# Performance work log

Measured on AMD Instinct MI355X. Metric: run time of the kernel, lower is better.

## Reference

```python
import jax, jax.numpy as jnp
import numpy as np
import math

T = 4096      # 2 s @ 2048 Hz (G2Net)
B = 64
NV = 16
SR = 2048.0
FLOW = 20.0
FHIGH = 512.0


def _build_wft():
    """Morlet-like wavelet filter bank in the frequency domain, exactly as in build()."""
    max_scale = T // (np.sqrt(2) * 2)
    if max_scale <= 1:
        max_scale = T // 2
    max_scale = np.floor(NV * np.log2(max_scale))
    scales = 2 * (2 ** (1 / NV)) ** np.arange(0, max_scale + 1)
    frequencies = SR * (6 / (2 * np.pi)) / scales
    frequencies = frequencies[frequencies >= FLOW]
    scales = scales[0:len(frequencies)]
    frequencies = frequencies[frequencies <= FHIGH]
    scales = scales[len(scales) - len(frequencies):len(scales)]
    padvalue = T // 2
    n = padvalue * 2 + T
    omega = np.arange(1, math.floor(n / 2) + 1, dtype=np.float64)
    omega = omega * (2 * np.pi) / n
    omega = np.concatenate((np.array([0.0]), omega,
                            -omega[np.arange(math.floor((n - 1) / 2), 0, -1, dtype=int) - 1]))
    wft = np.zeros([scales.size, omega.size])
    for jj, scale in enumerate(scales):
        expnt = -(scale * omega - 6) ** 2 / 2 * (omega > 0)
        wft[jj, :] = 2 * np.exp(expnt) * (omega > 0)
    return wft.astype(np.float32)  # [num_scales=75, n=8192]


def setup_inputs() -> dict:
    key = jax.random.key(0)
    inputs = jax.random.normal(key, (B, T), dtype=jnp.float32)
    wft = jnp.asarray(_build_wft())
    return {"inputs": inputs, "wft": wft}


def reference(inputs, wft):
    # inputs: [B, T] float32; wft: [S, n] float32 (n = 2*T)
    t = inputs.shape[1]
    pad = t // 2
    # symmetric (endpoint-including) reflect pad, same as tf.reverse of head/tail slices
    x = jnp.concatenate([inputs[:, :pad][:, ::-1], inputs, inputs[:, -pad:][:, ::-1]], axis=1)  # [B, n]
    f = jnp.fft.fft(x.astype(jnp.complex64), axis=-1)                   # [B, n]
    # kron(ones([S,1]), f) * wft  ==  broadcast multiply f[:,None,:] * wft[None]
    cwtcfs = jnp.fft.ifft(f[:, None, :] * wft.astype(jnp.complex64)[None, :, :], axis=-1)  # [B, S, n]
    return jnp.log(jnp.abs(cwtcfs[:, :, pad:pad + t]))                  # [B, S, T]
```

## Files before the change

### kernel.cpp

```cpp
#include <hip/hip_runtime.h>

#define TT 4096
#define NN 8192
#define NF 4096

#define SW(i) ((i) ^ ((((i) >> 4) ^ ((i) >> 8)) & 15))

typedef __attribute__((ext_vector_type(2))) float pf;

__device__ __forceinline__ float sin2pi(float x) { return __builtin_amdgcn_sinf(x); }
__device__ __forceinline__ float cos2pi(float x) { return __builtin_amdgcn_cosf(x); }

#define WMUL(ar, ai, br, bi) { float _t = (ar)*(br) - (ai)*(bi); \
                               (ai) = (ar)*(bi) + (ai)*(br); (ar) = _t; }

#define C32 0.9807852804032304f
#define S32 0.19509032201612825f

__device__ __constant__ const int PQ[16] =
    {0, 4, 8, 12, 1, 5, 9, 13, 2, 6, 10, 14, 3, 7, 11, 15};

template<int S, typename T>
__device__ __forceinline__ void dft4(T& ar, T& ai, T& br, T& bi,
                                     T& cr, T& ci, T& er, T& ei) {
    T t0r = ar + cr, t0i = ai + ci;
    T t1r = ar - cr, t1i = ai - ci;
    T t2r = br + er, t2i = bi + ei;
    T t3r = br - er, t3i = bi - ei;
    ar = t0r + t2r; ai = t0i + t2i;
    cr = t0r - t2r; ci = t0i - t2i;
    br = t1r - (float)S * t3i; bi = t1i + (float)S * t3r;
    er = t1r + (float)S * t3i; ei = t1i - (float)S * t3r;
}

template<int S, typename T>
__device__ __forceinline__ void tmuls16(T xr[16], T xi[16]) {
    const float C1 = 0.9238795325112867f;
    const float S1 = 0.3826834323650898f;
    const float R2 = 0.7071067811865476f;
    #define TM(idx, wr, wi) { T _r = xr[idx]*(wr) - xi[idx]*(wi); \
                              xi[idx] = xr[idx]*(wi) + xi[idx]*(wr); xr[idx] = _r; }
    TM(5,  C1,  (float)S * S1)
    TM(9,  R2,  (float)S * R2)
    TM(13, S1,  (float)S * C1)
    TM(6,  R2,  (float)S * R2)
    { T _r = -(float)S * xi[10]; xi[10] = (float)S * xr[10]; xr[10] = _r; }
    TM(14, -R2, (float)S * R2)
    TM(7,  S1,  (float)S * C1)
    TM(11, -R2, (float)S * R2)
    TM(15, -C1, -(float)S * S1)
    #undef TM
}

template<int S, typename T>
__device__ __forceinline__ void dft16_np(T xr[16], T xi[16]) {
    #pragma unroll
    for (int n0 = 0; n0 < 4; ++n0)
        dft4<S>(xr[n0], xi[n0], xr[n0 + 4], xi[n0 + 4],
                xr[n0 + 8], xi[n0 + 8], xr[n0 + 12], xi[n0 + 12]);

    tmuls16<S>(xr, xi);

    #pragma unroll
    for (int k0 = 0; k0 < 4; ++k0)
        dft4<S>(xr[4*k0], xi[4*k0], xr[4*k0+1], xi[4*k0+1],
                xr[4*k0+2], xi[4*k0+2], xr[4*k0+3], xi[4*k0+3]);
}

template<typename T>
__device__ __forceinline__ void twiddle16_p(T xr[16], T xi[16],
                                            float w1r, float w1i,
                                            float w8r, float w8i) {
    float wr = w1r, wi = w1i;
    #pragma unroll
    for (int q = 1; q < 16; ++q) {
        const int p = PQ[q];
        T _r = xr[p]*wr - xi[p]*wi;
        xi[p] = xr[p]*wi + xi[p]*wr; xr[p] = _r;
        if (q == 7) { wr = w8r; wi = w8i; }
        else        { WMUL(wr, wi, w1r, w1i) }
    }
}

template<int S, typename T>
__device__ __forceinline__ void dft16_mid8(T xr[16], T xi[16],
                                           T yr[8], T yi[8]) {
    #pragma unroll
    for (int n0 = 0; n0 < 4; ++n0)
        dft4<S>(xr[n0], xi[n0], xr[n0 + 4], xi[n0 + 4],
                xr[n0 + 8], xi[n0 + 8], xr[n0 + 12], xi[n0 + 12]);

    tmuls16<S>(xr, xi);

    #pragma unroll
    for (int k0 = 0; k0 < 4; ++k0) {
        T ar = xr[4*k0],     ai = xi[4*k0];
        T br = xr[4*k0 + 1], bi = xi[4*k0 + 1];
        T cr = xr[4*k0 + 2], ci = xi[4*k0 + 2];
        T er = xr[4*k0 + 3], ei = xi[4*k0 + 3];
        T t0r = ar + cr, t0i = ai + ci;
        T t1r = ar - cr, t1i = ai - ci;
        T t2r = br + er, t2i = bi + ei;
        T t3r = br - er, t3i = bi - ei;
        yr[k0]     = t1r - (float)S * t3i;  yi[k0]     = t1i + (float)S * t3r;
        yr[4 + k0] = t0r - t2r;             yi[4 + k0] = t0i - t2i;
    }
}

__device__ __forceinline__ int refl(int p) {
    if (p < 2048) return 2047 - p;
    if (p < 6144) return p - 2048;
    return 10239 - p;
}

__global__ __launch_bounds__(256) void fwd_kernel(const float* __restrict__ in,
                                                  float2* __restrict__ F) {
    __shared__ float2 lds[NF];
    const int b = blockIdx.x, tid = threadIdx.x;
    const int jj = tid & 15, h = tid >> 4, cx = jj ^ h;
    const float* row = in + b * TT;

    float xr[16], xi[16];

    #pragma unroll
    for (int r = 0; r < 16; ++r) {
        const int i = tid + 256 * r;
        xr[r] = row[refl(2 * i)];
        xi[r] = row[refl(2 * i + 1)];
    }
    dft16_np<-1>(xr, xi);
    twiddle16_p(xr, xi,
                cos2pi((float)tid * (1.0f / 4096.0f)), -sin2pi((float)tid * (1.0f / 4096.0f)),
                cos2pi((float)tid * (1.0f / 512.0f)),  -sin2pi((float)tid * (1.0f / 512.0f)));
    #pragma unroll
    for (int q = 0; q < 16; ++q)
        lds[(q << 8) + (h << 4) + (cx ^ q)] = make_float2(xr[PQ[q]], xi[PQ[q]]);
    __syncthreads();

    {
        #pragma unroll
        for (int q = 0; q < 16; ++q) {
            float2 v = lds[(h << 8) + (q << 4) + (cx ^ q)];
            xr[q] = v.x; xi[q] = v.y;
        }
        dft16_np<-1>(xr, xi);
        twiddle16_p(xr, xi,
                    cos2pi((float)jj * (1.0f / 256.0f)), -sin2pi((float)jj * (1.0f / 256.0f)),
                    cos2pi((float)jj * (1.0f / 32.0f)),  -sin2pi((float)jj * (1.0f / 32.0f)));
        #pragma unroll
        for (int q = 0; q < 16; ++q)
            lds[(h << 8) + (q << 4) + (cx ^ q)] = make_float2(xr[PQ[q]], xi[PQ[q]]);
    }
    __syncthreads();

    {
        #pragma unroll
        for (int q = 0; q < 16; ++q) {
            float2 v = lds[(h << 8) + (jj << 4) + (cx ^ q)];
            xr[q] = v.x; xi[q] = v.y;
        }
        dft16_np<-1>(xr, xi);
        __syncthreads();
        #pragma unroll
        for (int q = 0; q < 16; ++q)
            lds[(q << 8) + (jj << 4) + (cx ^ q)] = make_float2(xr[PQ[q]], xi[PQ[q]]);
    }
    __syncthreads();

    {
        const float c0 = cos2pi((float)(tid + 1) * (1.0f / 8192.0f));
        const float s0 = sin2pi((float)(tid + 1) * (1.0f / 8192.0f));
        float cc = c0, ss = s0;
        #pragma unroll
        for (int r = 0; r < 16; ++r) {
            const int i = tid + 256 * r;
            const int k = i + 1;
            const float2 za = lds[SW(k & (NF - 1))];
            const float2 zb = lds[SW((NF - k) & (NF - 1))];
            const float fer = 0.5f * (za.x + zb.x), fei = 0.5f * (za.y - zb.y);
            const float fo_r = 0.5f * (za.y + zb.y), fo_i = -0.5f * (za.x - zb.x);
            F[b * NF + i] = make_float2(fer + cc * fo_r + ss * fo_i,
                                        fei + cc * fo_i - ss * fo_r);
            if (r == 7) { cc = -s0; ss = c0; }
            else        { WMUL(cc, ss, C32, S32) }
        }
    }
}

__global__ __launch_bounds__(256) void inv_kernel(const float2* __restrict__ F,
                                                  const float* __restrict__ wft,
                                                  float* __restrict__ out,
                                                  int NS) {
    __shared__ pf lds[NF];
    const int blk = blockIdx.x;
    const int b = blk / NS;
    const int j = blk - b * NS;
    const int tid = threadIdx.x;
    const int jj = tid & 15, h = tid >> 4, cx = jj ^ h;

    const float2* Frow = F + b * NF;
    const float* wrow = wft + (size_t)j * NN + 1;
    float* orow = out + (size_t)(b * NS + j) * TT;
    const float LOGN = 9.0109131020007136f;
    const float HALF_LN2 = 0.34657359027997264f;

    pf xr[16], xi[16];

    {
        const float c0 = cos2pi((float)tid * (1.0f / 8192.0f));
        const float s0 = sin2pi((float)tid * (1.0f / 8192.0f));
        float cr = c0, ci = s0;
        #pragma unroll
        for (int r = 0; r < 16; ++r) {
            const int k = tid + 256 * r;
            const float2 f = Frow[k];
            const float w = wrow[k];
            const float d0r = f.x * w, d0i = f.y * w;
            pf vr, vi;
            vr.x = d0r;  vr.y = d0r * cr - d0i * ci;
            vi.x = d0i;  vi.y = d0r * ci + d0i * cr;
            xr[r] = vr;  xi[r] = vi;
            if (r == 7) { cr = -s0; ci = c0; }
            else        { WMUL(cr, ci, C32, S32) }
        }
    }
    dft16_np<1>(xr, xi);
    twiddle16_p(xr, xi,
                cos2pi((float)tid * (1.0f / 4096.0f)), sin2pi((float)tid * (1.0f / 4096.0f)),
                cos2pi((float)tid * (1.0f / 512.0f)),  sin2pi((float)tid * (1.0f / 512.0f)));

    #pragma unroll
    for (int q = 0; q < 16; ++q)
        lds[(q << 8) + (h << 4) + (cx ^ q)] = xr[PQ[q]];
    __syncthreads();
    #pragma unroll
    for (int q = 0; q < 16; ++q)
        xr[q] = lds[(h << 8) + (q << 4) + (cx ^ q)];
    __syncthreads();
    #pragma unroll
    for (int q = 0; q < 16; ++q)
        lds[(q << 8) + (h << 4) + (cx ^ q)] = xi[PQ[q]];
    __syncthreads();
    #pragma unroll
    for (int q = 0; q < 16; ++q)
        xi[q] = lds[(h << 8) + (q << 4) + (cx ^ q)];
    __syncthreads();

    dft16_np<1>(xr, xi);
    twiddle16_p(xr, xi,
                cos2pi((float)jj * (1.0f / 256.0f)), sin2pi((float)jj * (1.0f / 256.0f)),
                cos2pi((float)jj * (1.0f / 32.0f)),  sin2pi((float)jj * (1.0f / 32.0f)));

    #pragma unroll
    for (int q = 0; q < 16; ++q)
        lds[(h << 8) + (q << 4) + (cx ^ q)] = xr[PQ[q]];
    __syncthreads();
    #pragma unroll
    for (int q = 0; q < 16; ++q)
        xr[q] = lds[(jj << 8) + (h << 4) + (cx ^ q)];
    __syncthreads();
    #pragma unroll
    for (int q = 0; q < 16; ++q)
        lds[(h << 8) + (q << 4) + (cx ^ q)] = xi[PQ[q]];
    __syncthreads();
    #pragma unroll
    for (int q = 0; q < 16; ++q)
        xi[q] = lds[(jj << 8) + (h << 4) + (cx ^ q)];

    {
        pf yr[8], yi[8];
        dft16_mid8<1>(xr, xi, yr, yi);
        #pragma unroll
        for (int i2 = 0; i2 < 8; ++i2) {
            const pf m = yr[i2] * yr[i2] + yi[i2] * yi[i2];
            const float v0 = HALF_LN2 * __builtin_amdgcn_logf(m.x) - LOGN;
            const float v1 = HALF_LN2 * __builtin_amdgcn_logf(m.y) - LOGN;
            ((float2*)orow)[tid + 256 * i2] = make_float2(v0, v1);
        }
    }
}

extern "C" void kernel_launch(void* const* d_in, const int* in_sizes, int n_in,
                              void* d_out, int out_size, void* d_ws, size_t ws_size,
                              hipStream_t stream) {
    const float* inputs = (const float*)d_in[0];
    const float* wft = (const float*)d_in[1];
    float* out = (float*)d_out;

    const int B = in_sizes[0] / TT;
    const int NS = in_sizes[1] / NN;

    float2* F = (float2*)d_ws;

    hipLaunchKernelGGL(fwd_kernel, dim3(B), dim3(256), 0, stream, inputs, F);
    hipLaunchKernelGGL(inv_kernel, dim3(B * NS), dim3(256), 0, stream, F, wft, out, NS);
}
```

Before: 130.2 us.

## Fuse forward and inverse FFT kernels with per-batch flag synchronization

```diff
diff --git a/kernel.cpp b/kernel.cpp
--- a/kernel.cpp
+++ b/kernel.cpp
@@ -113,10 +113,8 @@
     return 10239 - p;
 }
 
-__global__ __launch_bounds__(256) void fwd_kernel(const float* __restrict__ in,
-                                                  float2* __restrict__ F) {
-    __shared__ float2 lds[NF];
-    const int b = blockIdx.x, tid = threadIdx.x;
+__device__ void fwd_body(const float* __restrict__ in, float2* __restrict__ F,
+                         float2* lds, int b, int tid) {
     const int jj = tid & 15, h = tid >> 4, cx = jj ^ h;
     const float* row = in + b * TT;
 
@@ -187,17 +185,10 @@
     }
 }
 
-__global__ __launch_bounds__(256) void inv_kernel(const float2* __restrict__ F,
-                                                  const float* __restrict__ wft,
-                                                  float* __restrict__ out,
-                                                  int NS) {
-    __shared__ pf lds[NF];
-    const int blk = blockIdx.x;
-    const int b = blk / NS;
-    const int j = blk - b * NS;
-    const int tid = threadIdx.x;
+__device__ void inv_body(const float2* __restrict__ F, const float* __restrict__ wft,
+                         float* __restrict__ out, pf* lds,
+                         int b, int j, int tid, int NS) {
     const int jj = tid & 15, h = tid >> 4, cx = jj ^ h;
-
     const float2* Frow = F + b * NF;
     const float* wrow = wft + (size_t)j * NN + 1;
     float* orow = out + (size_t)(b * NS + j) * TT;
@@ -280,6 +271,43 @@
     }
 }
 
+__global__ __launch_bounds__(256) void fused_kernel(const float* __restrict__ in,
+                                                    const float* __restrict__ wft,
+                                                    float* __restrict__ out,
+                                                    float2* __restrict__ F,
+                                                    unsigned* __restrict__ ctrl,
+                                                    int B, int NS) {
+    __shared__ pf lds[NF];
+    __shared__ unsigned s_t;
+    unsigned* flags = ctrl;
+    unsigned* counter = ctrl + 256;
+    const int tid = threadIdx.x;
+
+    if (tid == 0) s_t = atomicAdd(counter, 1u);
+    __syncthreads();
+    const unsigned t = s_t;
+
+    if (t < (unsigned)B) {
+        fwd_body(in, F, (float2*)lds, (int)t, tid);
+        __threadfence();
+        __syncthreads();
+        if (tid == 0)
+            __hip_atomic_store(&flags[t], 1u, __ATOMIC_RELEASE,
+                               __HIP_MEMORY_SCOPE_AGENT);
+    } else {
+        const unsigned p = t - (unsigned)B;
+        const int b = (int)(p / (unsigned)NS);
+        const int j = (int)(p - (unsigned)b * (unsigned)NS);
+        unsigned f;
+        do {
+            f = __hip_atomic_load(&flags[b], __ATOMIC_ACQUIRE,
+                                  __HIP_MEMORY_SCOPE_AGENT);
+            if (!f) __builtin_amdgcn_s_sleep(8);
+        } while (!f);
+        inv_body(F, wft, out, lds, b, j, tid, NS);
+    }
+}
+
 extern "C" void kernel_launch(void* const* d_in, const int* in_sizes, int n_in,
                               void* d_out, int out_size, void* d_ws, size_t ws_size,
                               hipStream_t stream) {
@@ -291,7 +319,9 @@
     const int NS = in_sizes[1] / NN;
 
     float2* F = (float2*)d_ws;
-
-    hipLaunchKernelGGL(fwd_kernel, dim3(B), dim3(256), 0, stream, inputs, F);
-    hipLaunchKernelGGL(inv_kernel, dim3(B * NS), dim3(256), 0, stream, F, wft, out, NS);
-}
+    unsigned* ctrl = (unsigned*)((char*)d_ws + (size_t)B * NF * sizeof(float2));
+
+    hipMemsetAsync(ctrl, 0, 2048, stream);
+    hipLaunchKernelGGL(fused_kernel, dim3(B + B * NS), dim3(256), 0, stream,
+                       inputs, wft, out, F, ctrl, B, NS);
+}
```

After: 348.6 us. 2.68x slower.
